# Kernel tuning notes

Measured on AMD Instinct MI355X. Metric: run time of the kernel, lower is better.

## Reference

```python
import jax, jax.numpy as jnp
import numpy as np

N = 20000      # nodes
E = 320000     # edges (avg degree 16)
IN = 128
HID = 64
CLS = 32
H0, H1, H2 = 4, 4, 6
SLOPE = 0.2


def _lin(key, fan_in, fan_out):
    kw, kb = jax.random.split(key)
    s = 1.0 / np.sqrt(fan_in)
    W = jax.random.uniform(kw, (fan_in, fan_out), minval=-s, maxval=s, dtype=jnp.float32)
    b = jax.random.uniform(kb, (fan_out,), minval=-s, maxval=s, dtype=jnp.float32)
    return W, b


def setup_inputs() -> dict:
    key = jax.random.key(0)
    ks = jax.random.split(key, 16)
    x = jax.random.normal(ks[0], (N, IN), dtype=jnp.float32)
    src = jax.random.randint(ks[1], (E,), 0, N)
    dst = jax.random.randint(ks[2], (E,), 0, N)
    W0s, b0s = _lin(ks[3], IN, H0 * HID)
    W0d, b0d = _lin(ks[4], IN, H0 * HID)
    a0 = jax.random.normal(ks[5], (H0, HID), dtype=jnp.float32) * 0.05
    d1 = H0 * HID  # 256, flattened hidden width
    W1s, b1s = _lin(ks[6], d1, H1 * HID)
    W1d, b1d = _lin(ks[7], d1, H1 * HID)
    a1 = jax.random.normal(ks[8], (H1, HID), dtype=jnp.float32) * 0.05
    W2s, b2s = _lin(ks[9], d1, H2 * CLS)
    W2d, b2d = _lin(ks[10], d1, H2 * CLS)
    a2 = jax.random.normal(ks[11], (H2, CLS), dtype=jnp.float32) * 0.05
    Wr2, br2 = _lin(ks[12], d1, H2 * CLS)  # residual projection (256 != 192)
    return dict(x=x, src=src, dst=dst,
                W0s=W0s, b0s=b0s, W0d=W0d, b0d=b0d, a0=a0,
                W1s=W1s, b1s=b1s, W1d=W1d, b1d=b1d, a1=a1,
                W2s=W2s, b2s=b2s, W2d=W2d, b2d=b2d, a2=a2,
                Wr2=Wr2, br2=br2)


def _gatv2_layer(x, src, dst, Ws, bs, Wd, bd, attn, heads, dim, res, act):
    n = x.shape[0]
    feat_src = (x @ Ws + bs).reshape(n, heads, dim)
    feat_dst = (x @ Wd + bd).reshape(n, heads, dim)
    # GATv2 edge scores: a^T LeakyReLU(W_l h_u + W_r h_v)
    e = jax.nn.leaky_relu(feat_src[src] + feat_dst[dst], SLOPE)  # [E,H,D]
    logits = jnp.einsum('ehd,hd->eh', e, attn)                    # [E,H]
    # numerically-stable edge softmax over incoming edges per destination
    m = jax.ops.segment_max(logits, dst, num_segments=n)
    m = jnp.where(jnp.isfinite(m), m, 0.0)
    ex = jnp.exp(logits - m[dst])
    denom = jax.ops.segment_sum(ex, dst, num_segments=n)
    alpha = ex / denom[dst]                                        # [E,H]
    out = jax.ops.segment_sum(feat_src[src] * alpha[:, :, None], dst, num_segments=n)
    if res == 'id':
        out = out + x.reshape(n, heads, dim)
    elif res is not None:
        Wr, br = res
        out = out + (x @ Wr + br).reshape(n, heads, dim)
    if act:
        out = jax.nn.elu(out)
    return out  # [n, heads, dim]


def reference(x, src, dst,
              W0s, b0s, W0d, b0d, a0,
              W1s, b1s, W1d, b1d, a1,
              W2s, b2s, W2d, b2d, a2,
              Wr2, br2):
    h = _gatv2_layer(x, src, dst, W0s, b0s, W0d, b0d, a0, H0, HID, None, True)
    h = h.reshape(N, H0 * HID)
    h = _gatv2_layer(h, src, dst, W1s, b1s, W1d, b1d, a1, H1, HID, 'id', True)
    h = h.reshape(N, H1 * HID)
    out = _gatv2_layer(h, src, dst, W2s, b2s, W2d, b2d, a2, H2, CLS, (Wr2, br2), False)
    return out.mean(axis=1)  # [N, num_classes]
```

## Files before the change

### kernel.cpp

```cpp
#include <hip/hip_runtime.h>
#include <hip/hip_bf16.h>
#include <float.h>
#include <math.h>

#define NN 20000
#define EE 320000
#define IN_DIM 128
#define DEG_CAP 64

typedef __attribute__((ext_vector_type(4))) float f32x4;
typedef _Float16 f16;
typedef __attribute__((ext_vector_type(2))) _Float16 f16x2;
typedef __attribute__((ext_vector_type(4))) _Float16 f16x4;
typedef __attribute__((ext_vector_type(8))) _Float16 f16x8;

__device__ __forceinline__ void prep_elem(const float* __restrict__ Wa, const float* __restrict__ ba, int na,
                                          const float* __restrict__ Wb, const float* __restrict__ bb, int nb,
                                          const float* __restrict__ Wc, const float* __restrict__ bc, int nc,
                                          int K, f16* __restrict__ Wt, float* __restrict__ bias_cat, int idx) {
    int n = idx / K;
    int k = idx - n * K;
    const float* W; const float* b; int nl; int ncols;
    if (n < na) { W = Wa; b = ba; nl = n; ncols = na; }
    else if (n < na + nb) { W = Wb; b = bb; nl = n - na; ncols = nb; }
    else { W = Wc; b = bc; nl = n - na - nb; ncols = nc; }
    Wt[(size_t)n * K + k] = (f16)W[(size_t)k * ncols + nl];
    if (k == 0) bias_cat[n] = b[nl];
}

#define SEG0 (512 * 128)
#define SEG1 (512 * 256)
#define SEG2 (576 * 256)
#define SEG3 (NN * IN_DIM / 4)
#define SEG4 (EE)
__global__ void prep_all(const float* __restrict__ W0s, const float* __restrict__ b0s,
                         const float* __restrict__ W0d, const float* __restrict__ b0d,
                         const float* __restrict__ W1s, const float* __restrict__ b1s,
                         const float* __restrict__ W1d, const float* __restrict__ b1d,
                         const float* __restrict__ W2s, const float* __restrict__ b2s,
                         const float* __restrict__ W2d, const float* __restrict__ b2d,
                         const float* __restrict__ Wr2, const float* __restrict__ br2,
                         const float* __restrict__ x,
                         const int* __restrict__ src, const int* __restrict__ dst,
                         f16* __restrict__ Wt0, float* __restrict__ bias0,
                         f16* __restrict__ Wt1, float* __restrict__ bias1,
                         f16* __restrict__ Wt2, float* __restrict__ bias2,
                         f16* __restrict__ A, unsigned int* __restrict__ deg,
                         int* __restrict__ csr_src) {
    int idx = blockIdx.x * 256 + threadIdx.x;
    if (idx < SEG0) {
        prep_elem(W0s, b0s, 256, W0d, b0d, 256, nullptr, nullptr, 0, 128, Wt0, bias0, idx);
    } else if ((idx -= SEG0) < SEG1) {
        prep_elem(W1s, b1s, 256, W1d, b1d, 256, nullptr, nullptr, 0, 256, Wt1, bias1, idx);
    } else if ((idx -= SEG1) < SEG2) {
        prep_elem(W2s, b2s, 192, W2d, b2d, 192, Wr2, br2, 192, 256, Wt2, bias2, idx);
    } else if ((idx -= SEG2) < SEG3) {
        float4 v = ((const float4*)x)[idx];
        f16x4 o = {(f16)v.x, (f16)v.y, (f16)v.z, (f16)v.w};
        ((f16x4*)A)[idx] = o;
    } else if ((idx -= SEG3) < SEG4) {
        int d = dst[idx];
        unsigned int pos = atomicAdd(&deg[d], 1u);
        if (pos < DEG_CAP) csr_src[(unsigned)d * DEG_CAP + pos] = src[idx];
    }
}

__global__ __launch_bounds__(256) void gemm_mfma_f16(
        const f16* __restrict__ A, const f16* __restrict__ Wt,
        const float* __restrict__ bias,
        f16* __restrict__ F0, f16* __restrict__ F1, float* __restrict__ F2,
        int b1, int b2, int M, int K, int S, int gx, int gy) {
    __shared__ f16 Bs[64 * 256];

    const int bid = blockIdx.x;
    const int p = bid & 7;
    const int q = bid >> 3;
    const int bn_i = q % gx;
    const int bm_i = (q / gx) * 8 + p;
    if (bm_i >= gy) return;
    const int bm = bm_i * 128;
    const int bn = bn_i * 64;

    const int tid = threadIdx.x;
    const int wave = tid >> 6;
    const int lane = tid & 63;
    const int m16 = lane & 15;
    const int quad = lane >> 4;

    {
        const int n = tid >> 2;
        const int q0 = tid & 3;
        for (int j = 0; j * 32 < K; ++j) {
            int k0 = j * 32 + q0 * 8;
            f16x8 v = *(const f16x8*)(Wt + (size_t)(bn + n) * K + k0);
            int chunk = (j * 4 + (n >> 4)) * 64 + q0 * 16 + (n & 15);
            *(f16x8*)&Bs[chunk * 8] = v;
        }
    }
    __syncthreads();

    const int rb0 = bm + wave * 32;
    f32x4 acc[2][4];
    #pragma unroll
    for (int mt = 0; mt < 2; ++mt)
        #pragma unroll
        for (int nt = 0; nt < 4; ++nt) acc[mt][nt] = (f32x4){0.f, 0.f, 0.f, 0.f};

    int ar[2];
    #pragma unroll
    for (int mt = 0; mt < 2; ++mt) {
        int row = rb0 + mt * 16 + m16;
        ar[mt] = row < M ? row : M - 1;
    }

    #pragma unroll 4
    for (int k0 = 0; k0 < K; k0 += 32) {
        f16x8 bs[4];
        #pragma unroll
        for (int nt = 0; nt < 4; ++nt)
            bs[nt] = *(const f16x8*)&Bs[(((k0 >> 5) * 4 + nt) * 64 + lane) * 8];
        f16x8 ah[2];
        #pragma unroll
        for (int mt = 0; mt < 2; ++mt)
            ah[mt] = *(const f16x8*)(A + (size_t)ar[mt] * K + k0 + quad * 8);
        #pragma unroll
        for (int nt = 0; nt < 4; ++nt)
            #pragma unroll
            for (int mt = 0; mt < 2; ++mt)
                acc[mt][nt] = __builtin_amdgcn_mfma_f32_16x16x32_f16(ah[mt], bs[nt], acc[mt][nt], 0, 0, 0);
    }

    __syncthreads();
    f16* Cs = Bs;

    if (bn < b2) {
        f16* __restrict__ Fb;
        int cs, cb;
        if (bn >= b1) { Fb = F1; cb = bn - b1; cs = b2 - b1; }
        else          { Fb = F0; cb = bn;      cs = b1; }
        f16* cw = Cs + wave * (32 * 66);
        #pragma unroll
        for (int nt = 0; nt < 4; ++nt) {
            float bv = bias[bn + nt * 16 + m16];
            #pragma unroll
            for (int mt = 0; mt < 2; ++mt)
                #pragma unroll
                for (int r = 0; r < 4; ++r) {
                    int row = mt * 16 + quad * 4 + r;
                    cw[row * 66 + nt * 16 + m16] = (f16)(acc[mt][nt][r] + bv);
                }
        }
        int lrow = lane >> 1;
        int lcol = (lane & 1) * 32;
        int grow = rb0 + lrow;
        if (grow < M) {
            #pragma unroll
            for (int j = 0; j < 4; ++j) {
                f16x8 v = *(f16x8*)&cw[lrow * 66 + lcol + j * 8];
                *(f16x8*)&Fb[(size_t)grow * cs + cb + lcol + j * 8] = v;
            }
        }
    } else {
        int cs = S - b2;
        #pragma unroll
        for (int nt = 0; nt < 4; ++nt) {
            int col = bn - b2 + nt * 16 + m16;
            float bv = bias[bn + nt * 16 + m16];
            #pragma unroll
            for (int mt = 0; mt < 2; ++mt)
                #pragma unroll
                for (int r = 0; r < 4; ++r) {
                    int row = rb0 + mt * 16 + quad * 4 + r;
                    if (row < M) F2[(size_t)row * cs + col] = acc[mt][nt][r] + bv;
                }
        }
    }
}

#define AGG_STEP4(U0)                                                         \
    _Pragma("unroll")                                                         \
    for (int uu = 0; uu < 4; ++uu) {                                          \
        const int u = (U0) + uu;                                              \
        const f16x8 cur = buf[u];                                             \
        unsigned su = (unsigned)cidx[u]; su = su < NN ? su : 0u;              \
        buf[u] = *(const f16x8*)&fsb[su * (unsigned)HD + off];                \
        cidx[u] = csr_src[max(min(jj0 + b + 16 + u, last), 0)];               \
        float pp = 0.f;                                                       \
        _Pragma("unroll")                                                     \
        for (int i = 0; i < 4; ++i) {                                         \
            f16x2 cp = (f16x2){cur[2 * i], cur[2 * i + 1]};                   \
            f16x2 xp = cp + fdp[i];                                           \
            unsigned xu = __builtin_bit_cast(unsigned, xp) & 0x7FFF7FFFu;     \
            f16x2 xa = __builtin_bit_cast(f16x2, xu);                         \
            pp = __builtin_amdgcn_fdot2(xp, a6p[i], pp, false);               \
            pp = __builtin_amdgcn_fdot2(xa, a4p[i], pp, false);               \
        }                                                                     \
        _Pragma("unroll")                                                     \
        for (int o = 1; o < GSZ; o <<= 1) pp += __shfl_xor(pp, o, 64);        \
        float w = (b + u < dg) ? __expf(pp) : 0.f;                            \
        lh += w;                                                              \
        _Pragma("unroll")                                                     \
        for (int d = 0; d < 8; ++d) acc[d] += w * (float)cur[d];              \
    }

template <int HD, int D, bool HAS_RES, bool DO_ELU, int OUT_MODE>
__global__ __launch_bounds__(256) void gat_node_aggregate(
        const f16* __restrict__ fsb, const f16* __restrict__ fdb,
        const float* __restrict__ attn,
        const unsigned int* __restrict__ degv,
        const int* __restrict__ csr_src,
        const float* __restrict__ resid, int RS,
        float* __restrict__ outF, f16* __restrict__ outA) {
    constexpr int LANES = HD / 8;
    constexpr int GSZ = D / 8;
    __shared__ float red[(OUT_MODE == 2) ? 8 : 1][(OUT_MODE == 2) ? HD : 1];

    const int wave = threadIdx.x >> 6;
    const int lane = threadIdx.x & 63;
    const int half = lane >> 5;
    const int ln = lane & 31;
    const int t = blockIdx.x * 8 + wave * 2 + half;
    const bool active = (ln < LANES);
    const unsigned off = active ? 8u * ln : 0u;

    f16x2 fdp[4], a6p[4], a4p[4];
    if (active) {
        f16x8 dv = *(const f16x8*)&fdb[(unsigned)t * HD + off];
        float4 aA = *(const float4*)&attn[off];
        float4 aB = *(const float4*)&attn[off + 4];
        float av[8] = {aA.x, aA.y, aA.z, aA.w, aB.x, aB.y, aB.z, aB.w};
        #pragma unroll
        for (int i = 0; i < 4; ++i) {
            fdp[i] = (f16x2){dv[2 * i], dv[2 * i + 1]};
            a6p[i] = (f16x2){(f16)(0.6f * av[2 * i]), (f16)(0.6f * av[2 * i + 1])};
            a4p[i] = (f16x2){(f16)(0.4f * av[2 * i]), (f16)(0.4f * av[2 * i + 1])};
        }
    } else {
        #pragma unroll
        for (int i = 0; i < 4; ++i) {
            fdp[i] = (f16x2){0, 0}; a6p[i] = (f16x2){0, 0}; a4p[i] = (f16x2){0, 0};
        }
    }

    const int jj0 = t * DEG_CAP;
    const int dg = min((int)degv[t], DEG_CAP);
    const int last = jj0 + dg - 1;
    const int degO = __shfl_xor(dg, 32, 64);
    const int mdeg = max(dg, degO);

    float acc[8];
    #pragma unroll
    for (int d = 0; d < 8; ++d) acc[d] = 0.f;
    float lh = 0.f;

    f16x8 buf[8];
    int cidx[8];
    #pragma unroll
    for (int u = 0; u < 8; ++u) {
        int e0 = max(min(jj0 + u, last), 0);
        unsigned s0 = (unsigned)csr_src[e0]; s0 = s0 < NN ? s0 : 0u;
        buf[u] = *(const f16x8*)&fsb[s0 * (unsigned)HD + off];
        cidx[u] = csr_src[max(min(jj0 + 8 + u, last), 0)];
    }

    for (int b = 0; b < mdeg; b += 8) {
        AGG_STEP4(0)
        if (b + 4 < mdeg) {
            AGG_STEP4(4)
        }
    }

    float inv = (lh > 0.f) ? 1.f / lh : 0.f;
    float vout[8];
    #pragma unroll
    for (int d = 0; d < 8; ++d) vout[d] = acc[d] * inv;
    if (HAS_RES && active) {
        float4 rA = *(const float4*)&resid[(unsigned)t * RS + off];
        float4 rB = *(const float4*)&resid[(unsigned)t * RS + off + 4];
        vout[0] += rA.x; vout[1] += rA.y; vout[2] += rA.z; vout[3] += rA.w;
        vout[4] += rB.x; vout[5] += rB.y; vout[6] += rB.z; vout[7] += rB.w;
    }
    if (DO_ELU) {
        #pragma unroll
        for (int d = 0; d < 8; ++d) vout[d] = vout[d] > 0.f ? vout[d] : expm1f(vout[d]);
    }

    if (OUT_MODE == 2) {
        const int nib = wave * 2 + half;
        if (active) {
            *(float4*)&red[nib][off] = make_float4(vout[0], vout[1], vout[2], vout[3]);
            *(float4*)&red[nib][off + 4] = make_float4(vout[4], vout[5], vout[6], vout[7]);
        }
        __syncthreads();
        int node = threadIdx.x >> 5;
        int col = threadIdx.x & 31;
        float ssum = 0.f;
        #pragma unroll
        for (int h = 0; h < 6; ++h) ssum += red[node][h * 32 + col];
        outF[(unsigned)(blockIdx.x * 8 + node) * 32 + col] = ssum * (1.f / 6.f);
    } else if (active) {
        f16x8 av;
        #pragma unroll
        for (int d = 0; d < 8; ++d) av[d] = (f16)vout[d];
        *(f16x8*)&outA[(unsigned)t * HD + off] = av;
        if (OUT_MODE == 0) {
            *(float4*)&outF[(unsigned)t * HD + off] = make_float4(vout[0], vout[1], vout[2], vout[3]);
            *(float4*)&outF[(unsigned)t * HD + off + 4] = make_float4(vout[4], vout[5], vout[6], vout[7]);
        }
    }
}

extern "C" void kernel_launch(void* const* d_in, const int* in_sizes, int n_in,
                              void* d_out, int out_size, void* d_ws, size_t ws_size,
                              hipStream_t stream) {
    const float* x   = (const float*)d_in[0];
    const int*   src = (const int*)d_in[1];
    const int*   dst = (const int*)d_in[2];
    const float* W0s = (const float*)d_in[3];
    const float* b0s = (const float*)d_in[4];
    const float* W0d = (const float*)d_in[5];
    const float* b0d = (const float*)d_in[6];
    const float* a0  = (const float*)d_in[7];
    const float* W1s = (const float*)d_in[8];
    const float* b1s = (const float*)d_in[9];
    const float* W1d = (const float*)d_in[10];
    const float* b1d = (const float*)d_in[11];
    const float* a1  = (const float*)d_in[12];
    const float* W2s = (const float*)d_in[13];
    const float* b2s = (const float*)d_in[14];
    const float* W2d = (const float*)d_in[15];
    const float* b2d = (const float*)d_in[16];
    const float* a2  = (const float*)d_in[17];
    const float* Wr2 = (const float*)d_in[18];
    const float* br2 = (const float*)d_in[19];

    f16* FsH = (f16*)d_ws;
    f16* FdH = FsH + (size_t)NN * 256;
    f16* A   = FdH + (size_t)NN * 256;
    float* O0 = (float*)(A + (size_t)NN * 256);
    f16* Wt0 = (f16*)(O0 + (size_t)NN * 256);
    f16* Wt1 = Wt0 + 512 * 128;
    f16* Wt2 = Wt1 + 512 * 256;
    float* bias0 = (float*)(Wt2 + 576 * 256);
    float* bias1 = bias0 + 512;
    float* bias2 = bias1 + 512;
    unsigned int* deg = (unsigned int*)(bias2 + 576);
    int* csr_src      = (int*)(deg + NN);

    hipMemsetAsync(deg, 0, (size_t)NN * 4, stream);
    {
        int total = SEG0 + SEG1 + SEG2 + SEG3 + SEG4;
        prep_all<<<(total + 255) / 256, 256, 0, stream>>>(
            W0s, b0s, W0d, b0d, W1s, b1s, W1d, b1d, W2s, b2s, W2d, b2d, Wr2, br2, x,
            src, dst, Wt0, bias0, Wt1, bias1, Wt2, bias2, A, deg, csr_src);
    }

    const int gy = (NN + 127) / 128;
    const int gy8 = ((gy + 7) / 8) * 8;
    const int nagg = NN / 8;

    gemm_mfma_f16<<<gy8 * 8, 256, 0, stream>>>(A, Wt0, bias0,
                                               FsH, FdH, nullptr, 256, 512, NN, 128, 512, 8, gy);
    gat_node_aggregate<256, 64, false, true, 0><<<nagg, 256, 0, stream>>>(
        FsH, FdH, a0, deg, csr_src, nullptr, 0, O0, A);

    gemm_mfma_f16<<<gy8 * 8, 256, 0, stream>>>(A, Wt1, bias1,
                                               FsH, FdH, nullptr, 256, 512, NN, 256, 512, 8, gy);
    gat_node_aggregate<256, 64, true, true, 1><<<nagg, 256, 0, stream>>>(
        FsH, FdH, a1, deg, csr_src, O0, 256, nullptr, A);

    gemm_mfma_f16<<<gy8 * 9, 256, 0, stream>>>(A, Wt2, bias2,
                                               FsH, FdH, O0, 192, 384, NN, 256, 576, 9, gy);
    gat_node_aggregate<192, 32, true, false, 2><<<nagg, 256, 0, stream>>>(
        FsH, FdH, a2, deg, csr_src, O0, 192, (float*)d_out, nullptr);
}
```

Before: 295.8 us.

## Fuse CSR build into first GEMM, stage CSR in LDS, async B loads

The edge-to-CSR scatter moves out of the prep kernel and into extra blocks of the first GEMM launch, so it overlaps with the matmul. The GEMM's weight tile is now loaded with global_load_lds direct-to-LDS copies instead of going through registers. Each aggregation block copies its 512 CSR entries into shared memory once, which drops the per-edge clamped global index loads. The aggregation loop also handles the leftover edges in steps of 2 rather than 4. The risks are a subtle LDS layout mismatch in the direct-load path and an added block-wide sync in the aggregation kernel.

```diff
diff --git a/kernel.cpp b/kernel.cpp
--- a/kernel.cpp
+++ b/kernel.cpp
@@ -13,6 +13,9 @@
 typedef __attribute__((ext_vector_type(2))) _Float16 f16x2;
 typedef __attribute__((ext_vector_type(4))) _Float16 f16x4;
 typedef __attribute__((ext_vector_type(8))) _Float16 f16x8;
+
+typedef const unsigned int __attribute__((address_space(1)))* gas_u32p;
+typedef unsigned int __attribute__((address_space(3)))* las_u32p;
 
 __device__ __forceinline__ void prep_elem(const float* __restrict__ Wa, const float* __restrict__ ba, int na,
                                           const float* __restrict__ Wb, const float* __restrict__ bb, int nb,
@@ -32,7 +35,6 @@
 #define SEG1 (512 * 256)
 #define SEG2 (576 * 256)
 #define SEG3 (NN * IN_DIM / 4)
-#define SEG4 (EE)
 __global__ void prep_all(const float* __restrict__ W0s, const float* __restrict__ b0s,
                          const float* __restrict__ W0d, const float* __restrict__ b0d,
                          const float* __restrict__ W1s, const float* __restrict__ b1s,
@@ -41,12 +43,10 @@
                          const float* __restrict__ W2d, const float* __restrict__ b2d,
                          const float* __restrict__ Wr2, const float* __restrict__ br2,
                          const float* __restrict__ x,
-                         const int* __restrict__ src, const int* __restrict__ dst,
                          f16* __restrict__ Wt0, float* __restrict__ bias0,
                          f16* __restrict__ Wt1, float* __restrict__ bias1,
                          f16* __restrict__ Wt2, float* __restrict__ bias2,
-                         f16* __restrict__ A, unsigned int* __restrict__ deg,
-                         int* __restrict__ csr_src) {
+                         f16* __restrict__ A) {
     int idx = blockIdx.x * 256 + threadIdx.x;
     if (idx < SEG0) {
         prep_elem(W0s, b0s, 256, W0d, b0d, 256, nullptr, nullptr, 0, 128, Wt0, bias0, idx);
@@ -58,10 +58,6 @@
         float4 v = ((const float4*)x)[idx];
         f16x4 o = {(f16)v.x, (f16)v.y, (f16)v.z, (f16)v.w};
         ((f16x4*)A)[idx] = o;
-    } else if ((idx -= SEG3) < SEG4) {
-        int d = dst[idx];
-        unsigned int pos = atomicAdd(&deg[d], 1u);
-        if (pos < DEG_CAP) csr_src[(unsigned)d * DEG_CAP + pos] = src[idx];
     }
 }
 
@@ -69,10 +65,22 @@
         const f16* __restrict__ A, const f16* __restrict__ Wt,
         const float* __restrict__ bias,
         f16* __restrict__ F0, f16* __restrict__ F1, float* __restrict__ F2,
-        int b1, int b2, int M, int K, int S, int gx, int gy) {
+        int b1, int b2, int M, int K, int S, int gx, int gy,
+        int GB, const int* __restrict__ esrc, const int* __restrict__ edst,
+        unsigned int* __restrict__ cursor, int* __restrict__ csr_dst, int E) {
     __shared__ f16 Bs[64 * 256];
 
     const int bid = blockIdx.x;
+    if (bid >= GB) {
+        int e = (bid - GB) * 256 + threadIdx.x;
+        if (e < E) {
+            int d = edst[e];
+            unsigned pos = atomicAdd(&cursor[d], 1u);
+            if (pos < DEG_CAP) csr_dst[(unsigned)d * DEG_CAP + pos] = esrc[e];
+        }
+        return;
+    }
+
     const int p = bid & 7;
     const int q = bid >> 3;
     const int bn_i = q % gx;
@@ -88,13 +96,13 @@
     const int quad = lane >> 4;
 
     {
-        const int n = tid >> 2;
-        const int q0 = tid & 3;
+        const f16* gs = Wt + (size_t)(bn + 16 * wave + (lane & 15)) * K + (lane >> 4) * 8;
+        #pragma unroll
         for (int j = 0; j * 32 < K; ++j) {
-            int k0 = j * 32 + q0 * 8;
-            f16x8 v = *(const f16x8*)(Wt + (size_t)(bn + n) * K + k0);
-            int chunk = (j * 4 + (n >> 4)) * 64 + q0 * 16 + (n & 15);
-            *(f16x8*)&Bs[chunk * 8] = v;
+            __builtin_amdgcn_global_load_lds(
+                (gas_u32p)(const void*)(gs + j * 32),
+                (las_u32p)(void*)(&Bs[((j * 4 + wave) * 64) * 8]),
+                16, 0, 0);
         }
     }
     __syncthreads();
@@ -177,14 +185,14 @@
     }
 }
 
-#define AGG_STEP4(U0)                                                         \
+#define AGG_STEP(U0, CNT)                                                     \
     _Pragma("unroll")                                                         \
-    for (int uu = 0; uu < 4; ++uu) {                                          \
+    for (int uu = 0; uu < (CNT); ++uu) {                                      \
         const int u = (U0) + uu;                                              \
         const f16x8 cur = buf[u];                                             \
         unsigned su = (unsigned)cidx[u]; su = su < NN ? su : 0u;              \
         buf[u] = *(const f16x8*)&fsb[su * (unsigned)HD + off];                \
-        cidx[u] = csr_src[max(min(jj0 + b + 16 + u, last), 0)];               \
+        cidx[u] = csr_l[nib64 + min(b + 16 + u, dgm1)];                       \
         float pp = 0.f;                                                       \
         _Pragma("unroll")                                                     \
         for (int i = 0; i < 4; ++i) {                                         \
@@ -213,7 +221,14 @@
         float* __restrict__ outF, f16* __restrict__ outA) {
     constexpr int LANES = HD / 8;
     constexpr int GSZ = D / 8;
+    __shared__ int csr_l[512];
     __shared__ float red[(OUT_MODE == 2) ? 8 : 1][(OUT_MODE == 2) ? HD : 1];
+
+    {
+        int i = threadIdx.x;
+        csr_l[i]       = csr_src[(size_t)blockIdx.x * 512 + i];
+        csr_l[i + 256] = csr_src[(size_t)blockIdx.x * 512 + i + 256];
+    }
 
     const int wave = threadIdx.x >> 6;
     const int lane = threadIdx.x & 63;
@@ -222,6 +237,7 @@
     const int t = blockIdx.x * 8 + wave * 2 + half;
     const bool active = (ln < LANES);
     const unsigned off = active ? 8u * ln : 0u;
+    const int nib64 = (wave * 2 + half) * 64;
 
     f16x2 fdp[4], a6p[4], a4p[4];
     if (active) {
@@ -242,9 +258,8 @@
         }
     }
 
-    const int jj0 = t * DEG_CAP;
     const int dg = min((int)degv[t], DEG_CAP);
-    const int last = jj0 + dg - 1;
+    const int dgm1 = max(dg - 1, 0);
     const int degO = __shfl_xor(dg, 32, 64);
     const int mdeg = max(dg, degO);
 
@@ -253,21 +268,29 @@
     for (int d = 0; d < 8; ++d) acc[d] = 0.f;
     float lh = 0.f;
 
+    __syncthreads();
+
     f16x8 buf[8];
     int cidx[8];
     #pragma unroll
     for (int u = 0; u < 8; ++u) {
-        int e0 = max(min(jj0 + u, last), 0);
-        unsigned s0 = (unsigned)csr_src[e0]; s0 = s0 < NN ? s0 : 0u;
+        unsigned s0 = (unsigned)csr_l[nib64 + min(u, dgm1)];
+        s0 = s0 < NN ? s0 : 0u;
         buf[u] = *(const f16x8*)&fsb[s0 * (unsigned)HD + off];
-        cidx[u] = csr_src[max(min(jj0 + 8 + u, last), 0)];
-    }
-
-    for (int b = 0; b < mdeg; b += 8) {
-        AGG_STEP4(0)
-        if (b + 4 < mdeg) {
-            AGG_STEP4(4)
-        }
+        cidx[u] = csr_l[nib64 + min(8 + u, dgm1)];
+    }
+
+    int b = 0;
+    for (; b + 8 <= mdeg; b += 8) {
+        AGG_STEP(0, 4)
+        AGG_STEP(4, 4)
+    }
+    {
+        const int rem = mdeg - b;
+        if (rem > 0) { AGG_STEP(0, 2) }
+        if (rem > 2) { AGG_STEP(2, 2) }
+        if (rem > 4) { AGG_STEP(4, 2) }
+        if (rem > 6) { AGG_STEP(6, 2) }
     }
 
     float inv = (lh > 0.f) ? 1.f / lh : 0.f;
@@ -349,28 +372,32 @@
 
     hipMemsetAsync(deg, 0, (size_t)NN * 4, stream);
     {
-        int total = SEG0 + SEG1 + SEG2 + SEG3 + SEG4;
+        int total = SEG0 + SEG1 + SEG2 + SEG3;
         prep_all<<<(total + 255) / 256, 256, 0, stream>>>(
             W0s, b0s, W0d, b0d, W1s, b1s, W1d, b1d, W2s, b2s, W2d, b2d, Wr2, br2, x,
-            src, dst, Wt0, bias0, Wt1, bias1, Wt2, bias2, A, deg, csr_src);
+            Wt0, bias0, Wt1, bias1, Wt2, bias2, A);
     }
 
     const int gy = (NN + 127) / 128;
     const int gy8 = ((gy + 7) / 8) * 8;
     const int nagg = NN / 8;
-
-    gemm_mfma_f16<<<gy8 * 8, 256, 0, stream>>>(A, Wt0, bias0,
-                                               FsH, FdH, nullptr, 256, 512, NN, 128, 512, 8, gy);
+    const int sblk = (EE + 255) / 256;
+
+    gemm_mfma_f16<<<gy8 * 8 + sblk, 256, 0, stream>>>(A, Wt0, bias0,
+                                               FsH, FdH, nullptr, 256, 512, NN, 128, 512, 8, gy,
+                                               gy8 * 8, src, dst, deg, csr_src, EE);
     gat_node_aggregate<256, 64, false, true, 0><<<nagg, 256, 0, stream>>>(
         FsH, FdH, a0, deg, csr_src, nullptr, 0, O0, A);
 
     gemm_mfma_f16<<<gy8 * 8, 256, 0, stream>>>(A, Wt1, bias1,
-                                               FsH, FdH, nullptr, 256, 512, NN, 256, 512, 8, gy);
+                                               FsH, FdH, nullptr, 256, 512, NN, 256, 512, 8, gy,
+                                               gy8 * 8, nullptr, nullptr, nullptr, nullptr, 0);
     gat_node_aggregate<256, 64, true, true, 1><<<nagg, 256, 0, stream>>>(
         FsH, FdH, a1, deg, csr_src, O0, 256, nullptr, A);
 
     gemm_mfma_f16<<<gy8 * 9, 256, 0, stream>>>(A, Wt2, bias2,
-                                               FsH, FdH, O0, 192, 384, NN, 256, 576, 9, gy);
+                                               FsH, FdH, O0, 192, 384, NN, 256, 576, 9, gy,
+                                               gy8 * 9, nullptr, nullptr, nullptr, nullptr, 0);
     gat_node_aggregate<192, 32, true, false, 2><<<nagg, 256, 0, stream>>>(
         FsH, FdH, a2, deg, csr_src, O0, 192, (float*)d_out, nullptr);
 }
```

After: 281.9 us. 4.7% less time.
